# Kernel tuning notes

Hardware: AMD Instinct MI355X
Metric: run time of the kernel (lower is better)

Reference implementation:

```python
import jax, jax.numpy as jnp
import numpy as np

B, C, H, W = 4, 64, 256, 256
HEADS = 4
HID = 128  # dim * ffn_expansion_factor
EPS = 1e-5


def _ln_chan(x, w, b):
    # LayerNorm over channel axis of [b,c,h,w] (equiv to to_3d -> LN over c -> to_4d)
    mu = x.mean(1, keepdims=True)
    var = jnp.mean((x - mu) ** 2, axis=1, keepdims=True)
    return (x - mu) / jnp.sqrt(var + EPS) * w[None, :, None, None] + b[None, :, None, None]


def _ln_last(x, w, b):
    mu = x.mean(-1, keepdims=True)
    var = jnp.mean((x - mu) ** 2, axis=-1, keepdims=True)
    return (x - mu) / jnp.sqrt(var + EPS) * w + b


def _conv1(x, Wt):
    # 1x1 conv, no bias; Wt: [out,in]
    return jnp.einsum('oi,bihw->bohw', Wt, x)


def _l2norm(x):
    # torch F.normalize(dim=-1): x / max(||x||, 1e-12)
    return x / jnp.maximum(jnp.linalg.norm(x, axis=-1, keepdims=True), 1e-12)


def _dct(inp1, inp2, Wq, Wk, Wv, temp):
    # Divide_Cross_Transformer: q from inp2, k/v from inp1; channel-wise attention
    b, c, h, w = inp1.shape
    ch = c // HEADS
    hw = h * w
    q = _conv1(inp2, Wq).reshape(b, HEADS, ch, hw)
    k = _conv1(inp1, Wk).reshape(b, HEADS, ch, hw)
    v = _conv1(inp1, Wv).reshape(b, HEADS, ch, hw)
    q = _l2norm(q)
    k = _l2norm(k)
    attn = jax.nn.softmax(jnp.einsum('bhcn,bhdn->bhcd', q, k) * temp[None], axis=-1)
    return attn, v  # attn: [b,head,ch,ch], v: [b,head,ch,hw]


def _ffn(x3, w1, b1, w2, b2):
    # torch nn.GELU default = exact erf
    hdn = jax.nn.gelu(jnp.einsum('bnc,hc->bnh', x3, w1) + b1, approximate=False)
    return jnp.einsum('bnh,ch->bnc', hdn, w2) + b2


def setup_inputs() -> dict:
    key = jax.random.key(0)
    ks = jax.random.split(key, 16)
    s = 0.05

    def n(k, shape):
        return jax.random.normal(k, shape, jnp.float32) * s

    ones = jnp.ones((C,), jnp.float32)
    zeros = jnp.zeros((C,), jnp.float32)
    return {
        'image': jax.random.normal(ks[0], (B, C, H, W), jnp.float32),
        'event': jax.random.normal(ks[1], (B, C, H, W), jnp.float32),
        'Wq_c': n(ks[2], (C, C)), 'Wk_c': n(ks[3], (C, C)), 'Wv_c': n(ks[4], (C, C)),
        'temp_c': jnp.ones((HEADS, 1, 1), jnp.float32),
        'Wq_d': n(ks[5], (C, C)), 'Wk_d': n(ks[6], (C, C)), 'Wv_d': n(ks[7], (C, C)),
        'temp_d': jnp.ones((HEADS, 1, 1), jnp.float32),
        'ln_img_w': ones, 'ln_img_b': zeros,
        'ln_evt_w': ones, 'ln_evt_b': zeros,
        'ln_com_w': ones, 'ln_com_b': zeros,
        'ln_dif_w': ones, 'ln_dif_b': zeros,
        'ln1_w': ones, 'ln1_b': zeros,
        'ln2_w': ones, 'ln2_b': zeros,
        'fc1c_w': n(ks[8], (HID, C)), 'fc1c_b': jnp.zeros((HID,), jnp.float32),
        'fc2c_w': n(ks[9], (C, HID)), 'fc2c_b': jnp.zeros((C,), jnp.float32),
        'fc1d_w': n(ks[10], (HID, C)), 'fc1d_b': jnp.zeros((HID,), jnp.float32),
        'fc2d_w': n(ks[11], (C, HID)), 'fc2d_b': jnp.zeros((C,), jnp.float32),
        'proj1_w': n(ks[12], (C, C)), 'proj2_w': n(ks[13], (C, C)),
    }


def reference(image, event, Wq_c, Wk_c, Wv_c, temp_c, Wq_d, Wk_d, Wv_d, temp_d,
              ln_img_w, ln_img_b, ln_evt_w, ln_evt_b, ln_com_w, ln_com_b,
              ln_dif_w, ln_dif_b, ln1_w, ln1_b, ln2_w, ln2_b,
              fc1c_w, fc1c_b, fc2c_w, fc2c_b, fc1d_w, fc1d_b, fc2d_w, fc2d_b,
              proj1_w, proj2_w):
    b, c, h, w = image.shape
    hw = h * w
    common = image + event
    differential = image - event

    ni = _ln_chan(image, ln_img_w, ln_img_b)
    ne = _ln_chan(event, ln_evt_w, ln_evt_b)
    nc = _ln_chan(common, ln_com_w, ln_com_b)
    nd = _ln_chan(differential, ln_dif_w, ln_dif_b)

    # common branch: shared conv weights (attn_common), attn maps multiplied
    a_ic, v_ic = _dct(ni, nc, Wq_c, Wk_c, Wv_c, temp_c)
    a_ec, v_ec = _dct(ne, nc, Wq_c, Wk_c, Wv_c, temp_c)
    a_c = a_ic * a_ec
    oc = jnp.einsum('bhcd,bhdn->bhcn', a_c, v_ic + v_ec)  # same attn for both matmuls
    oc = oc.reshape(b, c, h, w)
    oc = _conv1(oc, proj1_w)
    oc3 = oc.reshape(b, c, hw).transpose(0, 2, 1)  # b (hw) c
    oc3 = oc3 + _ffn(_ln_last(oc3, ln1_w, ln1_b), fc1c_w, fc1c_b, fc2c_w, fc2c_b)
    out_common = oc3.transpose(0, 2, 1).reshape(b, c, h, w)

    # differential branch: separate attn maps, not multiplied
    a_id, v_id = _dct(ni, nd, Wq_d, Wk_d, Wv_d, temp_d)
    a_ed, v_ed = _dct(ne, nd, Wq_d, Wk_d, Wv_d, temp_d)
    od = (jnp.einsum('bhcd,bhdn->bhcn', a_id, v_id)
          + jnp.einsum('bhcd,bhdn->bhcn', a_ed, v_ed))
    od = od.reshape(b, c, h, w)
    od = _conv1(od, proj2_w)
    od3 = od.reshape(b, c, hw).transpose(0, 2, 1)
    od3 = od3 + _ffn(_ln_last(od3, ln2_w, ln2_b), fc1d_w, fc1d_b, fc2d_w, fc2d_b)
    out_differential = od3.transpose(0, 2, 1).reshape(b, c, h, w)

    return (out_common, out_differential)
```

## Files before the change

### kernel.cpp

```cpp
#include <hip/hip_runtime.h>
#include <math.h>

typedef unsigned int u32;
typedef unsigned short u16;
typedef __attribute__((ext_vector_type(8))) short short8;
typedef __attribute__((ext_vector_type(4))) float float4v;

#define NBATCH 4
#define HW 65536

#define OFF_COV 0
#define OFF_T   131072
#define OFF_M   294912
#define OFF_P   344064
#define OFF_WC  393216
#define OFF_PAR 516096
#define WS_NEED ((size_t)(OFF_PAR + 1048576) * 4)

__device__ inline float bf2f(u16 h){ return __uint_as_float(((u32)h) << 16); }
__device__ inline u16 f2bf(float x){
  u32 u = __float_as_uint(x);
  u += 0x7fffu + ((u >> 16) & 1u);
  return (u16)(u >> 16);
}
__device__ inline u32 packbf2(float a, float b){
  u32 r;
  asm("v_cvt_pk_bf16_f32 %0, %1, %2" : "=v"(r) : "v"(a), "v"(b));
  return r;
}
__device__ inline float bfu(u32 u, int hi){
  return __uint_as_float(hi ? (u & 0xffff0000u) : (u << 16));
}

__device__ inline bool detect_f32(const void* probe, int t, int* s_cnt){
  if (t == 0) *s_cnt = 0;
  __syncthreads();
  u32 w = ((const u32*)probe)[t & 255];
  u32 ex = (w >> 7) & 0xffu;
  if (!(ex >= 113u && ex <= 133u)) atomicAdd(s_cnt, 1);
  __syncthreads();
  return *s_cnt >= 128;
}

__device__ inline bool detect_f32_512(const void* probe, int t, int* s_cnt){
  if (t == 0) *s_cnt = 0;
  __syncthreads();
  if (t < 256){
    u32 w = ((const u32*)probe)[t];
    u32 ex = (w >> 7) & 0xffu;
    if (!(ex >= 113u && ex <= 133u)) atomicAdd(s_cnt, 1);
  }
  __syncthreads();
  return *s_cnt >= 128;
}

__device__ inline void ld8(const u16* pb, const float* pf, size_t idx, bool f32, float* o){
  if (f32){
    const float4 a = *(const float4*)(pf + idx);
    const float4 b = *(const float4*)(pf + idx + 4);
    o[0]=a.x; o[1]=a.y; o[2]=a.z; o[3]=a.w; o[4]=b.x; o[5]=b.y; o[6]=b.z; o[7]=b.w;
  } else {
    uint4 r = *(const uint4*)(pb + idx);
    const u32* p = (const u32*)&r;
    #pragma unroll
    for (int j=0;j<8;j++) o[j] = bfu(p[j>>1], j&1);
  }
}

__device__ inline void softmax16(float* l){
  float m = l[0];
  #pragma unroll
  for (int i=1;i<16;i++) m = fmaxf(m, l[i]);
  float s = 0.f;
  #pragma unroll
  for (int i=0;i<16;i++){ l[i] = __expf(l[i]-m); s += l[i]; }
  float r = 1.0f/s;
  #pragma unroll
  for (int i=0;i<16;i++) l[i] *= r;
}

__global__ __launch_bounds__(256) void convert_all(
    const void* img,
    const void* t0, const void* t1, const void* t2, const void* t3,
    const void* t4, const void* t5, const void* t6, const void* t7,
    const void* t8, const void* t9, const void* t10, const void* t11,
    const void* t12, const void* t13, const void* t14, const void* t15,
    const void* t16, const void* t17, const void* t18, const void* t19,
    const void* t20, const void* t21, const void* t22, const void* t23,
    const void* t24, const void* t25, const void* t26, const void* t27,
    const void* t28, const void* t29,
    u16* __restrict__ wc)
{
  __shared__ int s_cnt;
  const int t = threadIdx.x;
  const bool f32 = detect_f32(img, t, &s_cnt);
  const int sizes[30] = {4096,4096,4096,4,4096,4096,4096,4,
                         64,64,64,64,64,64,64,64,64,64,64,64,
                         8192,128,8192,64,8192,128,8192,64,4096,4096};
  const void* srcs[30] = {t0,t1,t2,t3,t4,t5,t6,t7,t8,t9,t10,t11,t12,t13,t14,
                          t15,t16,t17,t18,t19,t20,t21,t22,t23,t24,t25,t26,t27,t28,t29};
  const int id = blockIdx.x;
  const void* s = srcs[id];
  const int n = sizes[id];
  u16* d = wc + (size_t)id*8192;
  for (int j = t; j < n; j += 256)
    d[j] = f32 ? f2bf(((const float*)s)[j]) : ((const u16*)s)[j];
}

__global__ __launch_bounds__(512, 4) void k1_cov(
    const void* __restrict__ img, const void* __restrict__ evt,
    const u16* __restrict__ lniw, const u16* __restrict__ lnib,
    const u16* __restrict__ lnew, const u16* __restrict__ lneb,
    const u16* __restrict__ lncw, const u16* __restrict__ lncb,
    const u16* __restrict__ lndw, const u16* __restrict__ lndb,
    float* __restrict__ cov, float* __restrict__ par, int use_par)
{
  __shared__ u16 NtL[4*64*72];
  __shared__ float spart[8][64][5];
  __shared__ float params[8][64];
  __shared__ int s_cnt;

  const int t = threadIdx.x;
  const bool f32 = detect_f32_512(img, t, &s_cnt);
  const u16* imgb = (const u16*)img; const float* imgf = (const float*)img;
  const u16* evtb = (const u16*)evt; const float* evtf = (const float*)evt;

  const int b = blockIdx.x >> 7;
  const int P0 = (blockIdx.x & 127) * 512;
  const int ch = t >> 3, pg = t & 7;
  const int wave = t >> 6, lane = t & 63, l15 = lane & 15, quad = lane >> 4;

  float wi=bf2f(lniw[ch]), bi=bf2f(lnib[ch]);
  float we=bf2f(lnew[ch]), be=bf2f(lneb[ch]);
  float wc_=bf2f(lncw[ch]), bc_=bf2f(lncb[ch]);
  float wd_=bf2f(lndw[ch]), bd_=bf2f(lndb[ch]);

  const int va = (wave==3)?0 : (wave==7)?1 : (wave<3)?2:3;
  const int vb = (wave==0)?2 : (wave==4)?3 :
                 ((wave==2)||(wave==6)||(wave==7))?1:0;

  float4v acc[4][4];
  #pragma unroll
  for (int i=0;i<4;i++)
    #pragma unroll
    for (int j=0;j<4;j++) acc[i][j]=(float4v)0.f;

  const size_t base = (size_t)(b*64 + ch) * HW;

  for (int it = 0; it < 8; ++it){
    const int p0 = P0 + it*64;
    float A[8], B[8];
    ld8(imgb, imgf, base + p0 + pg*8, f32, A);
    ld8(evtb, evtf, base + p0 + pg*8, f32, B);

    #pragma unroll 1
    for (int jp=0;jp<4;jp++){
      float xa=A[2*jp], xb=A[2*jp+1], ea=B[2*jp], eb=B[2*jp+1];
      float s0a=xa,     s0b=xb;
      float s1a=xa*xa,  s1b=xb*xb;
      float s2a=ea,     s2b=eb;
      float s3a=ea*ea,  s3b=eb*eb;
      float s4a=xa*ea,  s4b=xb*eb;
      #pragma unroll
      for (int m=8;m<=32;m<<=1){
        s0a+=__shfl_xor(s0a,m); s0b+=__shfl_xor(s0b,m);
        s1a+=__shfl_xor(s1a,m); s1b+=__shfl_xor(s1b,m);
        s2a+=__shfl_xor(s2a,m); s2b+=__shfl_xor(s2b,m);
        s3a+=__shfl_xor(s3a,m); s3b+=__shfl_xor(s3b,m);
        s4a+=__shfl_xor(s4a,m); s4b+=__shfl_xor(s4b,m);
      }
      if ((ch&7)==0){
        int px = pg*8 + 2*jp;
        spart[wave][px][0]=s0a; spart[wave][px][1]=s1a; spart[wave][px][2]=s2a;
        spart[wave][px][3]=s3a; spart[wave][px][4]=s4a;
        spart[wave][px+1][0]=s0b; spart[wave][px+1][1]=s1b; spart[wave][px+1][2]=s2b;
        spart[wave][px+1][3]=s3b; spart[wave][px+1][4]=s4b;
      }
    }
    __syncthreads();
    if (t < 64){
      float S0=0,S1=0,S2=0,S3=0,S4=0;
      #pragma unroll
      for (int w=0;w<8;w++){
        S0+=spart[w][t][0]; S1+=spart[w][t][1]; S2+=spart[w][t][2];
        S3+=spart[w][t][3]; S4+=spart[w][t][4];
      }
      const float inv = 0.015625f;
      float mu_i=S0*inv, mu_e=S2*inv;
      float r_i = rsqrtf(fmaf(S1,inv,-mu_i*mu_i)+1e-5f);
      float r_e = rsqrtf(fmaf(S3,inv,-mu_e*mu_e)+1e-5f);
      float mu_c=mu_i+mu_e, mu_d=mu_i-mu_e;
      float r_c = rsqrtf((S1+2.f*S4+S3)*inv - mu_c*mu_c + 1e-5f);
      float r_d = rsqrtf((S1-2.f*S4+S3)*inv - mu_d*mu_d + 1e-5f);
      params[0][t]=mu_i; params[1][t]=r_i; params[2][t]=mu_e; params[3][t]=r_e;
      params[4][t]=mu_c; params[5][t]=r_c; params[6][t]=mu_d; params[7][t]=r_d;
      if (use_par){
        float4 pv; pv.x=mu_i; pv.y=r_i; pv.z=mu_e; pv.w=r_e;
        *(float4*)(par + ((size_t)b*HW + p0 + t)*4) = pv;
      }
    }
    __syncthreads();

    {
      u32 u0[4], u1[4];
      #pragma unroll
      for (int jj=0;jj<4;jj++){
        int px = pg*8 + 2*jj;
        float2 mi01 = *(const float2*)&params[0][px];
        float2 ri01 = *(const float2*)&params[1][px];
        float2 me01 = *(const float2*)&params[2][px];
        float2 re01 = *(const float2*)&params[3][px];
        u0[jj] = packbf2(fmaf((A[2*jj]-mi01.x)*ri01.x, wi, bi),
                         fmaf((A[2*jj+1]-mi01.y)*ri01.y, wi, bi));
        u1[jj] = packbf2(fmaf((B[2*jj]-me01.x)*re01.x, we, be),
                         fmaf((B[2*jj+1]-me01.y)*re01.y, we, be));
      }
      *(uint4*)&NtL[(0*64+ch)*72 + pg*8] = make_uint4(u0[0],u0[1],u0[2],u0[3]);
      *(uint4*)&NtL[(1*64+ch)*72 + pg*8] = make_uint4(u1[0],u1[1],u1[2],u1[3]);
      #pragma unroll
      for (int jj=0;jj<4;jj++){
        int px = pg*8 + 2*jj;
        float2 mc01 = *(const float2*)&params[4][px];
        float2 rc01 = *(const float2*)&params[5][px];
        float2 md01 = *(const float2*)&params[6][px];
        float2 rd01 = *(const float2*)&params[7][px];
        float xc0=A[2*jj]+B[2*jj], xc1=A[2*jj+1]+B[2*jj+1];
        float xd0=A[2*jj]-B[2*jj], xd1=A[2*jj+1]-B[2*jj+1];
        u0[jj] = packbf2(fmaf((xc0-mc01.x)*rc01.x, wc_, bc_),
                         fmaf((xc1-mc01.y)*rc01.y, wc_, bc_));
        u1[jj] = packbf2(fmaf((xd0-md01.x)*rd01.x, wd_, bd_),
                         fmaf((xd1-md01.y)*rd01.y, wd_, bd_));
      }
      *(uint4*)&NtL[(2*64+ch)*72 + pg*8] = make_uint4(u0[0],u0[1],u0[2],u0[3]);
      *(uint4*)&NtL[(3*64+ch)*72 + pg*8] = make_uint4(u1[0],u1[1],u1[2],u1[3]);
    }
    __syncthreads();

    #pragma unroll
    for (int ks=0; ks<2; ks++){
      const int off = ks*32 + quad*8;
      short8 Af[4], Bf[4];
      #pragma unroll
      for (int mi=0;mi<4;mi++){
        Af[mi] = *(const short8*)&NtL[(va*64 + mi*16 + l15)*72 + off];
        Bf[mi] = *(const short8*)&NtL[(vb*64 + mi*16 + l15)*72 + off];
      }
      #pragma unroll
      for (int mi=0;mi<4;mi++)
        #pragma unroll
        for (int nj=0;nj<4;nj++)
          acc[mi][nj] = __builtin_amdgcn_mfma_f32_16x16x32_bf16(Af[mi], Bf[nj], acc[mi][nj], 0,0,0);
    }
  }
  float* cg = cov + ((size_t)wave*NBATCH + b)*4096;
  #pragma unroll
  for (int mi=0;mi<4;mi++)
    #pragma unroll
    for (int nj=0;nj<4;nj++){
      int row0 = mi*16 + quad*4, col = nj*16 + l15;
      #pragma unroll
      for (int r=0;r<4;r++)
        atomicAdd(&cg[(row0+r)*64 + col], acc[mi][nj][r]);
    }
}

__global__ __launch_bounds__(256) void p2a(
    const u16* __restrict__ Wq_c, const u16* __restrict__ Wk_c,
    const u16* __restrict__ Wq_d, const u16* __restrict__ Wk_d,
    float* __restrict__ ws)
{
  __shared__ float WL[64][65];
  __shared__ float CL[64][64];
  const int t = threadIdx.x;
  const int b = blockIdx.x & 3;
  const int which = blockIdx.x >> 2;
  int wsel, csel;
  switch (which){
    case 0: wsel=0; csel=0; break;
    case 1: wsel=1; csel=3; break;
    case 2: wsel=1; csel=7; break;
    case 3: wsel=2; csel=4; break;
    case 4: wsel=3; csel=3; break;
    case 5: wsel=3; csel=7; break;
    case 6: wsel=0; csel=1; break;
    case 7: wsel=0; csel=2; break;
    case 8: wsel=2; csel=5; break;
    default: wsel=2; csel=6; break;
  }
  const u16* W = (wsel==0)? Wq_c : (wsel==1)? Wk_c : (wsel==2)? Wq_d : Wk_d;
  const float* Cm = ws + ((size_t)csel*NBATCH + b)*4096;
  { int r = t>>2, c0 = (t&3)*16;
    #pragma unroll
    for (int i=0;i<16;i++) WL[r][c0+i] = bf2f(W[r*64 + c0 + i]);
    const float4* s = (const float4*)(Cm + r*64 + c0);
    float4* d = (float4*)&CL[r][c0];
    d[0]=s[0]; d[1]=s[1]; d[2]=s[2]; d[3]=s[3]; }
  __syncthreads();
  const int r = t>>2, k0 = (t&3)*16;
  float a[16];
  #pragma unroll
  for (int i=0;i<16;i++) a[i]=0.f;
  for (int m=0;m<64;m++){
    float wv = WL[r][m];
    #pragma unroll
    for (int i=0;i<16;i++) a[i] = fmaf(wv, CL[m][k0+i], a[i]);
  }
  float* o = ws + OFF_T + ((size_t)which*NBATCH + b)*4096 + r*64 + k0;
  #pragma unroll
  for (int i=0;i<16;i++) o[i] = a[i];
}

__global__ __launch_bounds__(256) void p2b(
    float* __restrict__ ws,
    const u16* __restrict__ Wq_c, const u16* __restrict__ Wk_c,
    const u16* __restrict__ Wq_d, const u16* __restrict__ Wk_d,
    const u16* __restrict__ Wv_c, const u16* __restrict__ Wv_d,
    const u16* __restrict__ temp_c, const u16* __restrict__ temp_d)
{
  const int b = blockIdx.x, t = threadIdx.x;
  __shared__ float rn[6][64];
  __shared__ float GLs[4][64][16];
  __shared__ float AL[3][64][16];
  const float* T = ws + OFF_T;
  {
    int s = t>>6, c = t&63;
    const float* Tp = T + ((size_t)s*NBATCH + b)*4096 + c*64;
    const u16* Wp = (s==0)? Wq_c : (s==3)? Wq_d : Wk_c;
    float acc=0;
    for (int k=0;k<64;k++) acc = fmaf(Tp[k], bf2f(Wp[c*64+k]), acc);
    rn[s][c] = 1.0f/fmaxf(sqrtf(fmaxf(acc,0.f)), 1e-12f);
    if (t < 128){
      int s2 = 4 + (t>>6);
      const float* Tp2 = T + ((size_t)s2*NBATCH + b)*4096 + c*64;
      float acc2=0;
      for (int k=0;k<64;k++) acc2 = fmaf(Tp2[k], bf2f(Wk_d[c*64+k]), acc2);
      rn[s2][c] = 1.0f/fmaxf(sqrtf(fmaxf(acc2,0.f)), 1e-12f);
    }
  }
  #pragma unroll 1
  for (int i=0;i<16;i++){
    int e = t*16 + i;
    int s = e >> 10, c = (e>>4)&63, dl = e&15, d = (c&~15)+dl;
    const float* Tp = T + ((size_t)(6+s)*NBATCH + b)*4096 + c*64;
    const u16* Wp = ((s<2)? Wk_c : Wk_d) + d*64;
    float acc=0;
    for (int j=0;j<64;j++) acc = fmaf(Tp[j], bf2f(Wp[j]), acc);
    GLs[s][c][dl] = acc;
  }
  __syncthreads();
  if (t < 192){
    int set = t>>6, c = t&63, h = c>>4, cb = c&~15;
    if (set == 0){
      float tc = bf2f(temp_c[h]);
      float rq = rn[0][c];
      float l1[16], l2[16];
      #pragma unroll
      for (int dl=0;dl<16;dl++){
        l1[dl] = GLs[0][c][dl]*rq*rn[1][cb+dl]*tc;
        l2[dl] = GLs[1][c][dl]*rq*rn[2][cb+dl]*tc;
      }
      softmax16(l1); softmax16(l2);
      #pragma unroll
      for (int dl=0;dl<16;dl++) AL[0][c][dl] = l1[dl]*l2[dl];
    } else {
      float td = bf2f(temp_d[h]);
      float rq = rn[3][c];
      int gi = (set==1)? 2 : 3;
      int rk = (set==1)? 4 : 5;
      float l[16];
      #pragma unroll
      for (int dl=0;dl<16;dl++) l[dl] = GLs[gi][c][dl]*rq*rn[rk][cb+dl]*td;
      softmax16(l);
      #pragma unroll
      for (int dl=0;dl<16;dl++) AL[set][c][dl] = l[dl];
    }
  }
  __syncthreads();
  for (int wsel=0; wsel<3; wsel++){
    const u16* Wv = (wsel==0)? Wv_c : Wv_d;
    #pragma unroll 1
    for (int i=0;i<16;i++){
      int e = t*16+i, c = e>>6, k = e&63, cb = c&~15;
      float acc=0;
      #pragma unroll
      for (int dl=0;dl<16;dl++) acc = fmaf(AL[wsel][c][dl], bf2f(Wv[(cb+dl)*64 + k]), acc);
      ws[OFF_M + ((size_t)wsel*NBATCH + b)*4096 + c*64 + k] = acc;
    }
  }
}

__global__ __launch_bounds__(256) void p2c(
    const u16* __restrict__ proj1, const u16* __restrict__ proj2,
    float* __restrict__ ws)
{
  __shared__ float WL[64][65];
  __shared__ float CL[64][64];
  const int t = threadIdx.x;
  const int b = blockIdx.x & 3;
  const int which = blockIdx.x >> 2;
  const u16* W = (which==0)? proj1 : proj2;
  const float* Cm = ws + OFF_M + ((size_t)which*NBATCH + b)*4096;
  { int r = t>>2, c0 = (t&3)*16;
    #pragma unroll
    for (int i=0;i<16;i++) WL[r][c0+i] = bf2f(W[r*64 + c0 + i]);
    const float4* s = (const float4*)(Cm + r*64 + c0);
    float4* d = (float4*)&CL[r][c0];
    d[0]=s[0]; d[1]=s[1]; d[2]=s[2]; d[3]=s[3]; }
  __syncthreads();
  const int r = t>>2, k0 = (t&3)*16;
  float a[16];
  #pragma unroll
  for (int i=0;i<16;i++) a[i]=0.f;
  for (int m=0;m<64;m++){
    float wv = WL[r][m];
    #pragma unroll
    for (int i=0;i<16;i++) a[i] = fmaf(wv, CL[m][k0+i], a[i]);
  }
  float* o = ws + OFF_P + ((size_t)which*NBATCH + b)*4096 + r*64 + k0;
  #pragma unroll
  for (int i=0;i<16;i++) o[i] = a[i];
}

__global__ __launch_bounds__(256) void k3_common(
    const void* __restrict__ img, const void* __restrict__ evt,
    const u16* __restrict__ lniw, const u16* __restrict__ lnib,
    const u16* __restrict__ lnew, const u16* __restrict__ lneb,
    const u16* __restrict__ ln1w, const u16* __restrict__ ln1b,
    const u16* __restrict__ fc1w, const u16* __restrict__ fc1b,
    const u16* __restrict__ fc2w, const u16* __restrict__ fc2b,
    const float* __restrict__ Pmat, void* __restrict__ outp, size_t obase,
    const float* __restrict__ par, int use_par)
{
  __shared__ u16 fc1L[128*72];
  __shared__ u16 fc2L[64*136];
  __shared__ u16 PcL[64*72];
  __shared__ u16 SB[64*136];
  __shared__ float spart[4][64][4];
  __shared__ float params[64][4];
  __shared__ float b1L[128];
  __shared__ float b2L[64];
  __shared__ int s_cnt;

  const int t = threadIdx.x;
  const bool f32 = detect_f32(img, t, &s_cnt);
  const u16* imgb = (const u16*)img; const float* imgf = (const float*)img;
  const u16* evtb = (const u16*)evt; const float* evtf = (const float*)evt;

  const int b = blockIdx.x >> 8;
  const int P0 = (blockIdx.x & 255) * 256;
  const int chg = t >> 3, pg = t & 7, ch0 = chg*2;
  const int wave = t >> 6, lane = t & 63, l15 = lane & 15, quad = lane >> 4;

  { int row = t >> 1, c0 = (t & 1)*32;
    const uint4* s = (const uint4*)(fc1w + row*64 + c0);
    uint4* d = (uint4*)&fc1L[row*72 + c0];
    d[0]=s[0]; d[1]=s[1]; d[2]=s[2]; d[3]=s[3]; }
  { int row = t >> 2, c0 = (t & 3)*32;
    const uint4* s = (const uint4*)(fc2w + row*128 + c0);
    uint4* d = (uint4*)&fc2L[row*136 + c0];
    d[0]=s[0]; d[1]=s[1]; d[2]=s[2]; d[3]=s[3]; }
  { int row = t >> 2, c0 = (t & 3)*16;
    const float* s = Pmat + (size_t)b*4096 + row*64 + c0;
    u32 u[8];
    #pragma unroll
    for (int i=0;i<8;i++) u[i] = packbf2(s[2*i], s[2*i+1]);
    uint4* d = (uint4*)&PcL[row*72 + c0];
    d[0] = make_uint4(u[0],u[1],u[2],u[3]);
    d[1] = make_uint4(u[4],u[5],u[6],u[7]); }
  if (t < 128) b1L[t] = bf2f(fc1b[t]);
  if (t < 64)  b2L[t] = bf2f(fc2b[t]);

  float wi0=bf2f(lniw[ch0]), wi1=bf2f(lniw[ch0+1]);
  float we0=bf2f(lnew[ch0]), we1=bf2f(lnew[ch0+1]);
  float bs0=bf2f(lnib[ch0]) + bf2f(lneb[ch0]);
  float bs1=bf2f(lnib[ch0+1]) + bf2f(lneb[ch0+1]);
  float w1r[4], b1r[4];
  #pragma unroll
  for (int nj=0;nj<4;nj++){ w1r[nj]=bf2f(ln1w[nj*16+l15]); b1r[nj]=bf2f(ln1b[nj*16+l15]); }
  __syncthreads();

  const size_t base_i = (size_t)(b*64 + ch0)*HW;
  for (int it=0; it<4; ++it){
    const int p0 = P0 + it*64;
    float A0[8], A1[8], B0[8], B1[8];
    ld8(imgb, imgf, base_i + p0 + pg*8, f32, A0);
    ld8(imgb, imgf, base_i + HW + p0 + pg*8, f32, A1);
    ld8(evtb, evtf, base_i + p0 + pg*8, f32, B0);
    ld8(evtb, evtf, base_i + HW + p0 + pg*8, f32, B1);

    if (use_par){
      const float4* pp = (const float4*)(par + ((size_t)b*HW + p0 + pg*8)*4);
      #pragma unroll
      for (int j=0;j<8;j++){
        float4 pr = pp[j];
        float a0=(A0[j]-pr.x)*pr.y, a1=(A1[j]-pr.x)*pr.y;
        float c0f=(B0[j]-pr.z)*pr.w, c1f=(B1[j]-pr.z)*pr.w;
        float n0 = fmaf(a0, wi0, fmaf(c0f, we0, bs0));
        float n1 = fmaf(a1, wi1, fmaf(c1f, we1, bs1));
        *(u32*)&SB[(pg*8+j)*136 + ch0] = packbf2(n0, n1);
      }
    } else {
      float si[8], sii[8], se[8], see[8];
      #pragma unroll
      for (int j=0;j<8;j++){
        float xi0=A0[j], xi1=A1[j], xe0=B0[j], xe1=B1[j];
        si[j]=xi0+xi1; sii[j]=fmaf(xi0,xi0,xi1*xi1);
        se[j]=xe0+xe1; see[j]=fmaf(xe0,xe0,xe1*xe1);
      }
      #pragma unroll
      for (int m=8;m<=32;m<<=1)
        #pragma unroll
        for (int j=0;j<8;j++){
          si[j]+=__shfl_xor(si[j],m); sii[j]+=__shfl_xor(sii[j],m);
          se[j]+=__shfl_xor(se[j],m); see[j]+=__shfl_xor(see[j],m);
        }
      if ((chg&7)==0){
        #pragma unroll
        for (int j=0;j<8;j++){
          spart[wave][pg*8+j][0]=si[j]; spart[wave][pg*8+j][1]=sii[j];
          spart[wave][pg*8+j][2]=se[j]; spart[wave][pg*8+j][3]=see[j];
        }
      }
      __syncthreads();
      if (t<64){
        float S0=0,S1=0,S2=0,S3=0;
        #pragma unroll
        for (int w=0;w<4;w++){ S0+=spart[w][t][0]; S1+=spart[w][t][1]; S2+=spart[w][t][2]; S3+=spart[w][t][3]; }
        const float inv=0.015625f;
        float mu_i=S0*inv, mu_e=S2*inv;
        float r_i=rsqrtf(fmaf(S1,inv,-mu_i*mu_i)+1e-5f);
        float r_e=rsqrtf(fmaf(S3,inv,-mu_e*mu_e)+1e-5f);
        params[t][0]=mu_i; params[t][1]=r_i; params[t][2]=mu_e; params[t][3]=r_e;
      }
      __syncthreads();
      #pragma unroll
      for (int j=0;j<8;j++){
        float4 pr = *(const float4*)&params[pg*8+j][0];
        float a0=(A0[j]-pr.x)*pr.y, a1=(A1[j]-pr.x)*pr.y;
        float c0f=(B0[j]-pr.z)*pr.w, c1f=(B1[j]-pr.z)*pr.w;
        float n0 = fmaf(a0, wi0, fmaf(c0f, we0, bs0));
        float n1 = fmaf(a1, wi1, fmaf(c1f, we1, bs1));
        *(u32*)&SB[(pg*8+j)*136 + ch0] = packbf2(n0, n1);
      }
    }
    __syncthreads();
    float4v acc1[4];
    #pragma unroll
    for (int nj=0;nj<4;nj++) acc1[nj]=(float4v)0.f;
    const int px_row = wave*16 + l15;
    #pragma unroll
    for (int ks=0;ks<2;ks++){
      const int off = ks*32 + quad*8;
      short8 af = *(const short8*)&SB[px_row*136 + off];
      #pragma unroll
      for (int nj=0;nj<4;nj++){
        short8 bw = *(const short8*)&PcL[(nj*16+l15)*72 + off];
        acc1[nj] = __builtin_amdgcn_mfma_f32_16x16x32_bf16(af, bw, acc1[nj], 0,0,0);
      }
    }
    float s[4], sq[4];
    #pragma unroll
    for (int j=0;j<4;j++){
      s[j] = acc1[0][j]+acc1[1][j]+acc1[2][j]+acc1[3][j];
      sq[j] = acc1[0][j]*acc1[0][j];
      sq[j] = fmaf(acc1[1][j],acc1[1][j],sq[j]);
      sq[j] = fmaf(acc1[2][j],acc1[2][j],sq[j]);
      sq[j] = fmaf(acc1[3][j],acc1[3][j],sq[j]);
    }
    #pragma unroll
    for (int m=1;m<=8;m<<=1)
      #pragma unroll
      for (int j=0;j<4;j++){ s[j]+=__shfl_xor(s[j],m); sq[j]+=__shfl_xor(sq[j],m); }
    float muj[4], rj[4];
    #pragma unroll
    for (int j=0;j<4;j++){
      muj[j]=s[j]*0.015625f;
      rj[j]=rsqrtf(fmaf(sq[j],0.015625f,-muj[j]*muj[j])+1e-5f);
    }
    #pragma unroll
    for (int nj=0;nj<4;nj++)
      #pragma unroll
      for (int j=0;j<4;j++){
        float tv = (acc1[nj][j]-muj[j])*rj[j];
        tv = fmaf(tv, w1r[nj], b1r[nj]);
        SB[(wave*16+quad*4+j)*136 + nj*16+l15] = f2bf(tv);
      }
    float4v accF[8];
    #pragma unroll
    for (int nh=0;nh<8;nh++) accF[nh]=(float4v)0.f;
    #pragma unroll
    for (int ks=0;ks<2;ks++){
      const int off = ks*32+quad*8;
      short8 af = *(const short8*)&SB[px_row*136 + off];
      #pragma unroll
      for (int nh=0;nh<8;nh++){
        short8 bw = *(const short8*)&fc1L[(nh*16+l15)*72 + off];
        accF[nh] = __builtin_amdgcn_mfma_f32_16x16x32_bf16(af, bw, accF[nh], 0,0,0);
      }
    }
    #pragma unroll
    for (int nh=0;nh<8;nh++){
      float bb = b1L[nh*16+l15];
      #pragma unroll
      for (int j=0;j<4;j++){
        float v = accF[nh][j] + bb;
        float g = 0.5f*v*(1.0f + erff(v*0.70710678118654752f));
        SB[(wave*16+quad*4+j)*136 + nh*16+l15] = f2bf(g);
      }
    }
    float4v accO[4];
    #pragma unroll
    for (int nj=0;nj<4;nj++) accO[nj]=(float4v)0.f;
    #pragma unroll
    for (int ks=0;ks<4;ks++){
      const int off = ks*32+quad*8;
      short8 ag = *(const short8*)&SB[px_row*136 + off];
      #pragma unroll
      for (int nj=0;nj<4;nj++){
        short8 bw = *(const short8*)&fc2L[(nj*16+l15)*136 + off];
        accO[nj] = __builtin_amdgcn_mfma_f32_16x16x32_bf16(ag, bw, accO[nj], 0,0,0);
      }
    }
    const int px0 = p0 + wave*16 + quad*4;
    #pragma unroll
    for (int nj=0;nj<4;nj++){
      float bb = b2L[nj*16+l15];
      int r = nj*16+l15;
      float v0 = acc1[nj][0] + accO[nj][0] + bb;
      float v1 = acc1[nj][1] + accO[nj][1] + bb;
      float v2 = acc1[nj][2] + accO[nj][2] + bb;
      float v3 = acc1[nj][3] + accO[nj][3] + bb;
      size_t oi = obase + (size_t)(b*64 + r)*HW + px0;
      if (f32){ float4 fv; fv.x=v0; fv.y=v1; fv.z=v2; fv.w=v3;
        *(float4*)((float*)outp + oi) = fv; }
      else *(uint2*)((u16*)outp + oi) = make_uint2(packbf2(v0,v1), packbf2(v2,v3));
    }
    __syncthreads();
  }
}

__global__ __launch_bounds__(256) void k3_diff(
    const void* __restrict__ img, const void* __restrict__ evt,
    const u16* __restrict__ lniw, const u16* __restrict__ lnib,
    const u16* __restrict__ lnew, const u16* __restrict__ lneb,
    const u16* __restrict__ ln2w, const u16* __restrict__ ln2b,
    const u16* __restrict__ fc1w, const u16* __restrict__ fc1b,
    const u16* __restrict__ fc2w, const u16* __restrict__ fc2b,
    const float* __restrict__ Pmat, void* __restrict__ outp, size_t obase,
    const float* __restrict__ par, int use_par)
{
  __shared__ u16 fc1L[128*72];
  __shared__ u16 fc2L[64*136];
  __shared__ u16 PiL[64*72];
  __shared__ u16 PeL[64*72];
  __shared__ u16 N2L[64*144];
  __shared__ float spart[4][64][4];
  __shared__ float params[64][4];
  __shared__ float b1L[128];
  __shared__ float b2L[64];
  __shared__ int s_cnt;

  const int t = threadIdx.x;
  const bool f32 = detect_f32(img, t, &s_cnt);
  const u16* imgb = (const u16*)img; const float* imgf = (const float*)img;
  const u16* evtb = (const u16*)evt; const float* evtf = (const float*)evt;

  const int b = blockIdx.x >> 8;
  const int P0 = (blockIdx.x & 255) * 256;
  const int chg = t >> 3, pg = t & 7, ch0 = chg*2;
  const int wave = t >> 6, lane = t & 63, l15 = lane & 15, quad = lane >> 4;

  { int row = t >> 1, c0 = (t & 1)*32;
    const uint4* s = (const uint4*)(fc1w + row*64 + c0);
    uint4* d = (uint4*)&fc1L[row*72 + c0];
    d[0]=s[0]; d[1]=s[1]; d[2]=s[2]; d[3]=s[3]; }
  { int row = t >> 2, c0 = (t & 3)*32;
    const uint4* s = (const uint4*)(fc2w + row*128 + c0);
    uint4* d = (uint4*)&fc2L[row*136 + c0];
    d[0]=s[0]; d[1]=s[1]; d[2]=s[2]; d[3]=s[3]; }
  { int row = t >> 2, c0 = (t & 3)*16;
    const float* si_ = Pmat + ((size_t)1*NBATCH + b)*4096 + row*64 + c0;
    const float* se_ = Pmat + ((size_t)2*NBATCH + b)*4096 + row*64 + c0;
    u32 u[8];
    #pragma unroll
    for (int i=0;i<8;i++) u[i] = packbf2(si_[2*i], si_[2*i+1]);
    uint4* d = (uint4*)&PiL[row*72 + c0];
    d[0] = make_uint4(u[0],u[1],u[2],u[3]); d[1] = make_uint4(u[4],u[5],u[6],u[7]);
    #pragma unroll
    for (int i=0;i<8;i++) u[i] = packbf2(se_[2*i], se_[2*i+1]);
    uint4* d2 = (uint4*)&PeL[row*72 + c0];
    d2[0] = make_uint4(u[0],u[1],u[2],u[3]); d2[1] = make_uint4(u[4],u[5],u[6],u[7]); }
  if (t < 128) b1L[t] = bf2f(fc1b[t]);
  if (t < 64)  b2L[t] = bf2f(fc2b[t]);

  float wi0=bf2f(lniw[ch0]), wi1=bf2f(lniw[ch0+1]);
  float bi0=bf2f(lnib[ch0]), bi1=bf2f(lnib[ch0+1]);
  float we0=bf2f(lnew[ch0]), we1=bf2f(lnew[ch0+1]);
  float be0=bf2f(lneb[ch0]), be1=bf2f(lneb[ch0+1]);
  float w1r[4], b1r[4];
  #pragma unroll
  for (int nj=0;nj<4;nj++){ w1r[nj]=bf2f(ln2w[nj*16+l15]); b1r[nj]=bf2f(ln2b[nj*16+l15]); }
  __syncthreads();

  const size_t base_i = (size_t)(b*64 + ch0)*HW;
  for (int it=0; it<4; ++it){
    const int p0 = P0 + it*64;
    float A0[8], A1[8], B0[8], B1[8];
    ld8(imgb, imgf, base_i + p0 + pg*8, f32, A0);
    ld8(imgb, imgf, base_i + HW + p0 + pg*8, f32, A1);
    ld8(evtb, evtf, base_i + p0 + pg*8, f32, B0);
    ld8(evtb, evtf, base_i + HW + p0 + pg*8, f32, B1);

    if (use_par){
      const float4* pp = (const float4*)(par + ((size_t)b*HW + p0 + pg*8)*4);
      #pragma unroll
      for (int j=0;j<8;j++){
        float4 pr = pp[j];
        float a0=(A0[j]-pr.x)*pr.y, a1=(A1[j]-pr.x)*pr.y;
        float c0f=(B0[j]-pr.z)*pr.w, c1f=(B1[j]-pr.z)*pr.w;
        *(u32*)&N2L[(pg*8+j)*144 + ch0]      = packbf2(fmaf(a0,wi0,bi0), fmaf(a1,wi1,bi1));
        *(u32*)&N2L[(pg*8+j)*144 + 72 + ch0] = packbf2(fmaf(c0f,we0,be0), fmaf(c1f,we1,be1));
      }
    } else {
      float si[8], sii[8], se[8], see[8];
      #pragma unroll
      for (int j=0;j<8;j++){
        float xi0=A0[j], xi1=A1[j], xe0=B0[j], xe1=B1[j];
        si[j]=xi0+xi1; sii[j]=fmaf(xi0,xi0,xi1*xi1);
        se[j]=xe0+xe1; see[j]=fmaf(xe0,xe0,xe1*xe1);
      }
      #pragma unroll
      for (int m=8;m<=32;m<<=1)
        #pragma unroll
        for (int j=0;j<8;j++){
          si[j]+=__shfl_xor(si[j],m); sii[j]+=__shfl_xor(sii[j],m);
          se[j]+=__shfl_xor(se[j],m); see[j]+=__shfl_xor(see[j],m);
        }
      if ((chg&7)==0){
        #pragma unroll
        for (int j=0;j<8;j++){
          spart[wave][pg*8+j][0]=si[j]; spart[wave][pg*8+j][1]=sii[j];
          spart[wave][pg*8+j][2]=se[j]; spart[wave][pg*8+j][3]=see[j];
        }
      }
      __syncthreads();
      if (t<64){
        float S0=0,S1=0,S2=0,S3=0;
        #pragma unroll
        for (int w=0;w<4;w++){ S0+=spart[w][t][0]; S1+=spart[w][t][1]; S2+=spart[w][t][2]; S3+=spart[w][t][3]; }
        const float inv=0.015625f;
        float mu_i=S0*inv, mu_e=S2*inv;
        float r_i=rsqrtf(fmaf(S1,inv,-mu_i*mu_i)+1e-5f);
        float r_e=rsqrtf(fmaf(S3,inv,-mu_e*mu_e)+1e-5f);
        params[t][0]=mu_i; params[t][1]=r_i; params[t][2]=mu_e; params[t][3]=r_e;
      }
      __syncthreads();
      #pragma unroll
      for (int j=0;j<8;j++){
        float4 pr = *(const float4*)&params[pg*8+j][0];
        float a0=(A0[j]-pr.x)*pr.y, a1=(A1[j]-pr.x)*pr.y;
        float c0f=(B0[j]-pr.z)*pr.w, c1f=(B1[j]-pr.z)*pr.w;
        *(u32*)&N2L[(pg*8+j)*144 + ch0]      = packbf2(fmaf(a0,wi0,bi0), fmaf(a1,wi1,bi1));
        *(u32*)&N2L[(pg*8+j)*144 + 72 + ch0] = packbf2(fmaf(c0f,we0,be0), fmaf(c1f,we1,be1));
      }
    }
    __syncthreads();
    float4v acc1[4];
    #pragma unroll
    for (int nj=0;nj<4;nj++) acc1[nj]=(float4v)0.f;
    const int px_row = wave*16 + l15;
    #pragma unroll
    for (int ks=0;ks<2;ks++){
      const int off = ks*32 + quad*8;
      short8 ai = *(const short8*)&N2L[px_row*144 + off];
      short8 ae = *(const short8*)&N2L[px_row*144 + 72 + off];
      #pragma unroll
      for (int nj=0;nj<4;nj++){
        short8 bwi = *(const short8*)&PiL[(nj*16+l15)*72 + off];
        acc1[nj] = __builtin_amdgcn_mfma_f32_16x16x32_bf16(ai, bwi, acc1[nj], 0,0,0);
        short8 bwe = *(const short8*)&PeL[(nj*16+l15)*72 + off];
        acc1[nj] = __builtin_amdgcn_mfma_f32_16x16x32_bf16(ae, bwe, acc1[nj], 0,0,0);
      }
    }
    float s[4], sq[4];
    #pragma unroll
    for (int j=0;j<4;j++){
      s[j] = acc1[0][j]+acc1[1][j]+acc1[2][j]+acc1[3][j];
      sq[j] = acc1[0][j]*acc1[0][j];
      sq[j] = fmaf(acc1[1][j],acc1[1][j],sq[j]);
      sq[j] = fmaf(acc1[2][j],acc1[2][j],sq[j]);
      sq[j] = fmaf(acc1[3][j],acc1[3][j],sq[j]);
    }
    #pragma unroll
    for (int m=1;m<=8;m<<=1)
      #pragma unroll
      for (int j=0;j<4;j++){ s[j]+=__shfl_xor(s[j],m); sq[j]+=__shfl_xor(sq[j],m); }
    float muj[4], rj[4];
    #pragma unroll
    for (int j=0;j<4;j++){
      muj[j]=s[j]*0.015625f;
      rj[j]=rsqrtf(fmaf(sq[j],0.015625f,-muj[j]*muj[j])+1e-5f);
    }
    #pragma unroll
    for (int nj=0;nj<4;nj++)
      #pragma unroll
      for (int j=0;j<4;j++){
        float tv = (acc1[nj][j]-muj[j])*rj[j];
        tv = fmaf(tv, w1r[nj], b1r[nj]);
        N2L[(wave*16+quad*4+j)*144 + nj*16+l15] = f2bf(tv);
      }
    float4v accF[8];
    #pragma unroll
    for (int nh=0;nh<8;nh++) accF[nh]=(float4v)0.f;
    #pragma unroll
    for (int ks=0;ks<2;ks++){
      const int off = ks*32+quad*8;
      short8 af = *(const short8*)&N2L[px_row*144 + off];
      #pragma unroll
      for (int nh=0;nh<8;nh++){
        short8 bw = *(const short8*)&fc1L[(nh*16+l15)*72 + off];
        accF[nh] = __builtin_amdgcn_mfma_f32_16x16x32_bf16(af, bw, accF[nh], 0,0,0);
      }
    }
    #pragma unroll
    for (int nh=0;nh<8;nh++){
      float bb = b1L[nh*16+l15];
      #pragma unroll
      for (int j=0;j<4;j++){
        float v = accF[nh][j] + bb;
        float g = 0.5f*v*(1.0f + erff(v*0.70710678118654752f));
        N2L[(wave*16+quad*4+j)*144 + nh*16+l15] = f2bf(g);
      }
    }
    float4v accO[4];
    #pragma unroll
    for (int nj=0;nj<4;nj++) accO[nj]=(float4v)0.f;
    #pragma unroll
    for (int ks=0;ks<4;ks++){
      const int off = ks*32+quad*8;
      short8 ag = *(const short8*)&N2L[px_row*144 + off];
      #pragma unroll
      for (int nj=0;nj<4;nj++){
        short8 bw = *(const short8*)&fc2L[(nj*16+l15)*136 + off];
        accO[nj] = __builtin_amdgcn_mfma_f32_16x16x32_bf16(ag, bw, accO[nj], 0,0,0);
      }
    }
    const int px0 = p0 + wave*16 + quad*4;
    #pragma unroll
    for (int nj=0;nj<4;nj++){
      float bb = b2L[nj*16+l15];
      int r = nj*16+l15;
      float v0 = acc1[nj][0] + accO[nj][0] + bb;
      float v1 = acc1[nj][1] + accO[nj][1] + bb;
      float v2 = acc1[nj][2] + accO[nj][2] + bb;
      float v3 = acc1[nj][3] + accO[nj][3] + bb;
      size_t oi = obase + (size_t)(b*64 + r)*HW + px0;
      if (f32){ float4 fv; fv.x=v0; fv.y=v1; fv.z=v2; fv.w=v3;
        *(float4*)((float*)outp + oi) = fv; }
      else *(uint2*)((u16*)outp + oi) = make_uint2(packbf2(v0,v1), packbf2(v2,v3));
    }
    __syncthreads();
  }
}

extern "C" void kernel_launch(void* const* d_in, const int* in_sizes, int n_in,
                              void* d_out, int out_size, void* d_ws, size_t ws_size,
                              hipStream_t stream)
{
  const void* img = d_in[0];
  const void* evt = d_in[1];
  float* ws = (float*)d_ws;
  u16* wc = (u16*)(ws + OFF_WC);
  float* par = ws + OFF_PAR;
  const int use_par = (ws_size >= WS_NEED) ? 1 : 0;
  #define SLOT(i) (wc + (size_t)((i)-2)*8192)

  hipMemsetAsync(ws, 0, 131072*sizeof(float), stream);
  convert_all<<<dim3(30), dim3(256), 0, stream>>>(img,
      d_in[2], d_in[3], d_in[4], d_in[5], d_in[6], d_in[7], d_in[8], d_in[9],
      d_in[10], d_in[11], d_in[12], d_in[13], d_in[14], d_in[15], d_in[16], d_in[17],
      d_in[18], d_in[19], d_in[20], d_in[21], d_in[22], d_in[23], d_in[24], d_in[25],
      d_in[26], d_in[27], d_in[28], d_in[29], d_in[30], d_in[31], wc);
  k1_cov<<<dim3(512), dim3(512), 0, stream>>>(img, evt,
      SLOT(10), SLOT(11), SLOT(12), SLOT(13), SLOT(14), SLOT(15), SLOT(16), SLOT(17),
      ws, par, use_par);
  p2a<<<dim3(40), dim3(256), 0, stream>>>(SLOT(2), SLOT(3), SLOT(6), SLOT(7), ws);
  p2b<<<dim3(4), dim3(256), 0, stream>>>(ws, SLOT(2), SLOT(3), SLOT(6), SLOT(7),
      SLOT(4), SLOT(8), SLOT(5), SLOT(9));
  p2c<<<dim3(12), dim3(256), 0, stream>>>(SLOT(30), SLOT(31), ws);
  k3_common<<<dim3(1024), dim3(256), 0, stream>>>(img, evt,
      SLOT(10), SLOT(11), SLOT(12), SLOT(13), SLOT(18), SLOT(19),
      SLOT(22), SLOT(23), SLOT(24), SLOT(25), ws + OFF_P, d_out, (size_t)0, par, use_par);
  k3_diff<<<dim3(1024), dim3(256), 0, stream>>>(img, evt,
      SLOT(10), SLOT(11), SLOT(12), SLOT(13), SLOT(20), SLOT(21),
      SLOT(26), SLOT(27), SLOT(28), SLOT(29), ws + OFF_P, d_out, (size_t)16777216, par, use_par);
  #undef SLOT
}
```

Measured before the change: 567.9 us.

## Replicate covariance accumulators, prefetch inputs, and use DPP/permlane channel reductions

The covariance kernel now loads the next 64-pixel chunk of image and event while the current one is processed. The xor-shuffle reductions across channels are replaced with DPP row_xmask and permlane16/32 swap instructions. Atomic covariance accumulation is spread over 8 replica buffers chosen by block index to cut atomic contention, and p2a sums the replicas. This costs an extra memset, extra workspace, and more reads in p2a, and is only active when the workspace is large enough.

```diff
diff --git a/kernel.cpp b/kernel.cpp
--- a/kernel.cpp
+++ b/kernel.cpp
@@ -15,7 +15,9 @@
 #define OFF_P   344064
 #define OFF_WC  393216
 #define OFF_PAR 516096
+#define OFF_COVR 1564672
 #define WS_NEED ((size_t)(OFF_PAR + 1048576) * 4)
+#define WS_NEED_REP ((size_t)(OFF_COVR + 7*131072) * 4)
 
 __device__ inline float bf2f(u16 h){ return __uint_as_float(((u32)h) << 16); }
 __device__ inline u16 f2bf(float x){
@@ -31,6 +33,22 @@
 __device__ inline float bfu(u32 u, int hi){
   return __uint_as_float(hi ? (u & 0xffff0000u) : (u << 16));
 }
+
+__device__ inline float xor8_sum(float v){
+  int t = __builtin_amdgcn_mov_dpp(__float_as_int(v), 0x128, 0xf, 0xf, true);
+  return v + __int_as_float(t);
+}
+__device__ inline float xor16_sum(float v){
+  float x = v, y = v;
+  asm("v_permlane16_swap_b32 %0, %1" : "+v"(x), "+v"(y));
+  return x + y;
+}
+__device__ inline float xor32_sum(float v){
+  float x = v, y = v;
+  asm("v_permlane32_swap_b32 %0, %1" : "+v"(x), "+v"(y));
+  return x + y;
+}
+__device__ inline float redch(float v){ return xor32_sum(xor16_sum(xor8_sum(v))); }
 
 __device__ inline bool detect_f32(const void* probe, int t, int* s_cnt){
   if (t == 0) *s_cnt = 0;
@@ -113,7 +131,8 @@
     const u16* __restrict__ lnew, const u16* __restrict__ lneb,
     const u16* __restrict__ lncw, const u16* __restrict__ lncb,
     const u16* __restrict__ lndw, const u16* __restrict__ lndb,
-    float* __restrict__ cov, float* __restrict__ par, int use_par)
+    float* __restrict__ cov, float* __restrict__ covext,
+    float* __restrict__ par, int use_par, int use_rep)
 {
   __shared__ u16 NtL[4*64*72];
   __shared__ float spart[8][64][5];
@@ -147,28 +166,25 @@
 
   const size_t base = (size_t)(b*64 + ch) * HW;
 
+  float A[8], B[8], An[8], Bn[8];
+  ld8(imgb, imgf, base + P0 + pg*8, f32, A);
+  ld8(evtb, evtf, base + P0 + pg*8, f32, B);
+
   for (int it = 0; it < 8; ++it){
     const int p0 = P0 + it*64;
-    float A[8], B[8];
-    ld8(imgb, imgf, base + p0 + pg*8, f32, A);
-    ld8(evtb, evtf, base + p0 + pg*8, f32, B);
+    if (it < 7){
+      ld8(imgb, imgf, base + p0 + 64 + pg*8, f32, An);
+      ld8(evtb, evtf, base + p0 + 64 + pg*8, f32, Bn);
+    }
 
     #pragma unroll 1
     for (int jp=0;jp<4;jp++){
       float xa=A[2*jp], xb=A[2*jp+1], ea=B[2*jp], eb=B[2*jp+1];
-      float s0a=xa,     s0b=xb;
-      float s1a=xa*xa,  s1b=xb*xb;
-      float s2a=ea,     s2b=eb;
-      float s3a=ea*ea,  s3b=eb*eb;
-      float s4a=xa*ea,  s4b=xb*eb;
-      #pragma unroll
-      for (int m=8;m<=32;m<<=1){
-        s0a+=__shfl_xor(s0a,m); s0b+=__shfl_xor(s0b,m);
-        s1a+=__shfl_xor(s1a,m); s1b+=__shfl_xor(s1b,m);
-        s2a+=__shfl_xor(s2a,m); s2b+=__shfl_xor(s2b,m);
-        s3a+=__shfl_xor(s3a,m); s3b+=__shfl_xor(s3b,m);
-        s4a+=__shfl_xor(s4a,m); s4b+=__shfl_xor(s4b,m);
-      }
+      float s0a=redch(xa),          s0b=redch(xb);
+      float s1a=redch(xa*xa),       s1b=redch(xb*xb);
+      float s2a=redch(ea),          s2b=redch(eb);
+      float s3a=redch(ea*ea),       s3b=redch(eb*eb);
+      float s4a=redch(xa*ea),       s4b=redch(xb*eb);
       if ((ch&7)==0){
         int px = pg*8 + 2*jp;
         spart[wave][px][0]=s0a; spart[wave][px][1]=s1a; spart[wave][px][2]=s2a;
@@ -251,8 +267,12 @@
         for (int nj=0;nj<4;nj++)
           acc[mi][nj] = __builtin_amdgcn_mfma_f32_16x16x32_bf16(Af[mi], Bf[nj], acc[mi][nj], 0,0,0);
     }
-  }
-  float* cg = cov + ((size_t)wave*NBATCH + b)*4096;
+    #pragma unroll
+    for (int j=0;j<8;j++){ A[j]=An[j]; B[j]=Bn[j]; }
+  }
+  const int rep = use_rep ? (blockIdx.x & 7) : 0;
+  float* cbase = (rep==0) ? cov : (covext + (size_t)(rep-1)*131072);
+  float* cg = cbase + ((size_t)wave*NBATCH + b)*4096;
   #pragma unroll
   for (int mi=0;mi<4;mi++)
     #pragma unroll
@@ -267,7 +287,7 @@
 __global__ __launch_bounds__(256) void p2a(
     const u16* __restrict__ Wq_c, const u16* __restrict__ Wk_c,
     const u16* __restrict__ Wq_d, const u16* __restrict__ Wk_d,
-    float* __restrict__ ws)
+    float* __restrict__ ws, int use_rep)
 {
   __shared__ float WL[64][65];
   __shared__ float CL[64][64];
@@ -288,13 +308,25 @@
     default: wsel=2; csel=6; break;
   }
   const u16* W = (wsel==0)? Wq_c : (wsel==1)? Wk_c : (wsel==2)? Wq_d : Wk_d;
-  const float* Cm = ws + ((size_t)csel*NBATCH + b)*4096;
+  const size_t coff = ((size_t)csel*NBATCH + b)*4096;
+  const float* Cm = ws + coff;
+  const float* Ce = ws + OFF_COVR;
   { int r = t>>2, c0 = (t&3)*16;
     #pragma unroll
     for (int i=0;i<16;i++) WL[r][c0+i] = bf2f(W[r*64 + c0 + i]);
-    const float4* s = (const float4*)(Cm + r*64 + c0);
-    float4* d = (float4*)&CL[r][c0];
-    d[0]=s[0]; d[1]=s[1]; d[2]=s[2]; d[3]=s[3]; }
+    #pragma unroll
+    for (int i=0;i<4;i++){
+      float4 v = *(const float4*)(Cm + r*64 + c0 + i*4);
+      if (use_rep){
+        #pragma unroll
+        for (int rr=0; rr<7; rr++){
+          const float4 w2 = *(const float4*)(Ce + (size_t)rr*131072 + coff + r*64 + c0 + i*4);
+          v.x+=w2.x; v.y+=w2.y; v.z+=w2.z; v.w+=w2.w;
+        }
+      }
+      *(float4*)&CL[r][c0 + i*4] = v;
+    }
+  }
   __syncthreads();
   const int r = t>>2, k0 = (t&3)*16;
   float a[16];
@@ -872,10 +904,14 @@
   float* ws = (float*)d_ws;
   u16* wc = (u16*)(ws + OFF_WC);
   float* par = ws + OFF_PAR;
+  float* covext = ws + OFF_COVR;
   const int use_par = (ws_size >= WS_NEED) ? 1 : 0;
+  const int use_rep = (ws_size >= WS_NEED_REP) ? 1 : 0;
   #define SLOT(i) (wc + (size_t)((i)-2)*8192)
 
   hipMemsetAsync(ws, 0, 131072*sizeof(float), stream);
+  if (use_rep)
+    hipMemsetAsync(covext, 0, (size_t)7*131072*sizeof(float), stream);
   convert_all<<<dim3(30), dim3(256), 0, stream>>>(img,
       d_in[2], d_in[3], d_in[4], d_in[5], d_in[6], d_in[7], d_in[8], d_in[9],
       d_in[10], d_in[11], d_in[12], d_in[13], d_in[14], d_in[15], d_in[16], d_in[17],
@@ -883,8 +919,8 @@
       d_in[26], d_in[27], d_in[28], d_in[29], d_in[30], d_in[31], wc);
   k1_cov<<<dim3(512), dim3(512), 0, stream>>>(img, evt,
       SLOT(10), SLOT(11), SLOT(12), SLOT(13), SLOT(14), SLOT(15), SLOT(16), SLOT(17),
-      ws, par, use_par);
-  p2a<<<dim3(40), dim3(256), 0, stream>>>(SLOT(2), SLOT(3), SLOT(6), SLOT(7), ws);
+      ws, covext, par, use_par, use_rep);
+  p2a<<<dim3(40), dim3(256), 0, stream>>>(SLOT(2), SLOT(3), SLOT(6), SLOT(7), ws, use_rep);
   p2b<<<dim3(4), dim3(256), 0, stream>>>(ws, SLOT(2), SLOT(3), SLOT(6), SLOT(7),
       SLOT(4), SLOT(8), SLOT(5), SLOT(9));
   p2c<<<dim3(12), dim3(256), 0, stream>>>(SLOT(30), SLOT(31), ws);
```

Result: slower. 581.8 us (+2.4%).
